# Performance work log

Measured on AMD Instinct MI355X. Metric: run time of the kernel, lower is better.

Reference implementation:

```python
import jax, jax.numpy as jnp
import numpy as np

B, L, H, NH = 2, 512, 128, 2
DH = H // NH
POS_VOCAB, REL_VOCAB = 512, 257


def setup_inputs() -> dict:
    key = jax.random.key(0)
    ks = jax.random.split(key, 16)
    s = 0.02
    inp = {
        "query": jax.random.normal(ks[0], (B, L, H), jnp.float32),
        "key": jax.random.normal(ks[1], (B, L, H), jnp.float32),
        "value": jax.random.normal(ks[2], (B, L, H), jnp.float32),
        "Wq": jax.random.normal(ks[3], (H, H), jnp.float32) * s,
        "bq": jnp.zeros((H,), jnp.float32),
        "Wk": jax.random.normal(ks[4], (H, H), jnp.float32) * s,
        "bk": jnp.zeros((H,), jnp.float32),
        "Wv": jax.random.normal(ks[5], (H, H), jnp.float32) * s,
        "bv": jnp.zeros((H,), jnp.float32),
        "Wo": jax.random.normal(ks[6], (H, H), jnp.float32) * s,
        "bo": jnp.zeros((H,), jnp.float32),
        "E_PK": jax.random.normal(ks[7], (POS_VOCAB, H), jnp.float32) * s,
        "E_PV": jax.random.normal(ks[8], (POS_VOCAB, H), jnp.float32) * s,
        "E_RK": jax.random.normal(ks[9], (REL_VOCAB, H), jnp.float32) * s,
        "E_RV": jax.random.normal(ks[10], (REL_VOCAB, H), jnp.float32) * s,
        "poss_seq": jax.random.randint(ks[11], (B, L), 0, POS_VOCAB),
        "interval_seq": jax.random.randint(ks[12], (B, L, L), 0, REL_VOCAB),
        # causal mask (True = attend), same role as attn_mask in the torch module
        "attn_mask": jnp.broadcast_to(jnp.tril(jnp.ones((L, L), bool)), (B, L, L)),
    }
    return inp


def reference(query, key, value, Wq, bq, Wk, bk, Wv, bv, Wo, bo,
              E_PK, E_PV, E_RK, E_RV, poss_seq, interval_seq, attn_mask):
    b, l, _ = query.shape
    # linear projections (torch Linear: x @ W.T + b)
    Q = query @ Wq.T + bq
    K = key @ Wk.T + bk + E_PK[poss_seq]
    V = value @ Wv.T + bv + E_PV[poss_seq]
    # relative key/value embeddings: (b, l, l, h, dh) -> (b, h, l, l, dh)
    rel_k = E_RK[interval_seq].reshape(b, l, l, NH, DH).transpose(0, 3, 1, 2, 4)
    rel_v = E_RV[interval_seq].reshape(b, l, l, NH, DH).transpose(0, 3, 1, 2, 4)
    # split heads: (b, h, l, dh)
    Qh = Q.reshape(b, l, NH, DH).transpose(0, 2, 1, 3)
    Kh = K.reshape(b, l, NH, DH).transpose(0, 2, 1, 3)
    Vh = V.reshape(b, l, NH, DH).transpose(0, 2, 1, 3)
    scores = jnp.einsum('bhld,bhkd->bhlk', Qh, Kh)
    scores = scores + jnp.einsum('bhld,bhlkd->bhlk', Qh, rel_k)
    scores = scores / jnp.sqrt(jnp.float32(DH))
    m = attn_mask[:, None]  # (b, 1, l, l)
    scores = jnp.where(m, scores, -jnp.inf)
    w = jax.nn.softmax(scores, axis=-1)
    w = jnp.where(m, w, 0.0)
    out = jnp.einsum('bhlk,bhkd->bhld', w, Vh)
    out = out + jnp.einsum('bhlk,bhlkd->bhld', w, rel_v)
    out = out.transpose(0, 2, 1, 3).reshape(b, l, H)
    out = out @ Wo.T + bo
    out = jnp.where(jnp.isnan(out), 0.0, out)
    return out
```

## Files before the change

### kernel.cpp

```cpp
#include <hip/hip_runtime.h>
#include <math.h>

#define LL 512
#define HH 128
#define NHH 2
#define DHH 64
#define RELV 257

#define OFF_QH   0
#define OFF_KT   131072
#define OFF_VH   262144
#define OFF_PK   393216
#define OFF_WQT  919552
#define OFF_WKT  935936
#define OFF_WVT  952320
#define OFF_WOT  968704
#define OFF_ERKT 985088

__global__ void prep_kernel(const float* Wq, const float* Wk, const float* Wv,
                            const float* Wo, const float* E_RK, float* ws) {
    int g = blockIdx.x * 256 + threadIdx.x;
    if (g < 65536) {
        int m = g >> 14, rem = g & 16383, i = rem >> 7, j = rem & 127;
        const float* W = (m == 0) ? Wq : (m == 1) ? Wk : (m == 2) ? Wv : Wo;
        ws[OFF_WQT + m * 16384 + i * 128 + j] = W[j * 128 + i];
    } else if (g < 65536 + 128 * RELV) {
        int g2 = g - 65536;
        int hd = g2 / RELV, r = g2 - hd * RELV;
        ws[OFF_ERKT + hd * RELV + r] = E_RK[r * HH + hd];
    }
}

__launch_bounds__(256)
__global__ void qkv_kernel(const float* q_in, const float* k_in, const float* v_in,
                           const float* bq, const float* bk, const float* bv,
                           const float* E_PK, const float* E_PV, const int* poss,
                           const float* Wqt, const float* Wkt, const float* Wvt,
                           const float* ERKt,
                           float* Qh, float* Kt, float* Vh, float* PK) {
    int row = blockIdx.x;
    int b = row >> 9, l = row & 511;
    int t = threadIdx.x;
    int j = t & 127, half = t >> 7;

    __shared__ float xin[3][128];
    __shared__ float pp[3][2][128];
    __shared__ float qrow[128];

    for (int g = t; g < 384; g += 256) {
        int m = g >> 7, i = g & 127;
        const float* src = (m == 0) ? q_in : (m == 1) ? k_in : v_in;
        xin[m][i] = src[row * 128 + i];
    }
    __syncthreads();

    float aq = 0.f, ak = 0.f, av = 0.f;
    int i0 = half * 64;
#pragma unroll 8
    for (int i = i0; i < i0 + 64; i++) {
        float xq = xin[0][i], xk = xin[1][i], xv = xin[2][i];
        aq += xq * Wqt[i * 128 + j];
        ak += xk * Wkt[i * 128 + j];
        av += xv * Wvt[i * 128 + j];
    }
    pp[0][half][j] = aq; pp[1][half][j] = ak; pp[2][half][j] = av;
    __syncthreads();

    if (t < 128) {
        int pos = poss[row];
        float q = pp[0][0][j] + pp[0][1][j] + bq[j];
        float k = pp[1][0][j] + pp[1][1][j] + bk[j] + E_PK[pos * 128 + j];
        float v = pp[2][0][j] + pp[2][1][j] + bv[j] + E_PV[pos * 128 + j];
        int h = j >> 6, d = j & 63, bh = b * NHH + h;
        Qh[(bh * LL + l) * DHH + d] = q;
        Vh[(bh * LL + l) * DHH + d] = v;
        Kt[(bh * DHH + d) * LL + l] = k;
        qrow[j] = q;
    }
    __syncthreads();

    int h = t >> 7, rr = t & 127;
    const float* qh = qrow + h * DHH;
    for (int r = rr; r < RELV; r += 128) {
        float acc = 0.f;
        const float* er = ERKt + h * DHH * RELV + r;
#pragma unroll 8
        for (int dd = 0; dd < DHH; dd++) acc += qh[dd] * er[dd * RELV];
        PK[((b * NHH + h) * LL + l) * RELV + r] = acc;
    }
}

__launch_bounds__(256)
__global__ void attn_kernel(const float* Qh, const float* Kt, const float* Vh,
                            const float* PK, const float* E_RV,
                            const float* Wot, const float* bo,
                            const int* interval, float* out) {
    int blk = blockIdx.x;
    int b = blk & 1;
    int l = 511 - (blk >> 1);
    int t = threadIdx.x;
    int w = t >> 6, lane = t & 63;
    int h = w >> 1, kseg = w & 1;
    int bh = b * NHH + h;
    int nk = l + 1;
    int kmid = (((nk + 1) >> 1) + 3) & ~3;
    int kbase = kseg ? kmid : 0;
    int kend  = kseg ? nk : (kmid < nk ? kmid : nk);

    __shared__ float q4[4][DHH];
    __shared__ float pks[4][RELV];
    __shared__ float wb[4][RELV];
    __shared__ __align__(16) float sc[4][256];
    __shared__ float oa[4][DHH];
    __shared__ float po[2][HH];
    __shared__ float reds[4];

    q4[w][lane] = Qh[(bh * LL + l) * DHH + lane];
    const float* PKrow = PK + (bh * LL + l) * RELV;
#pragma unroll
    for (int c = 0; c < 4; c++) {
        pks[w][lane + c * 64] = PKrow[lane + c * 64];
        wb[w][lane + c * 64] = 0.f;
    }
    if (lane == 0) { pks[w][256] = PKrow[256]; wb[w][256] = 0.f; }
    __syncthreads();

    int k0 = kbase + lane * 4;
    float4 a4 = make_float4(0.f, 0.f, 0.f, 0.f);
    int4 idx4 = make_int4(0, 0, 0, 0);
    const int* idxr = interval + (b * LL + l) * LL;
    if (k0 < kend) {
        idx4 = ((const int4*)idxr)[k0 >> 2];
        const float* kb = Kt + bh * DHH * LL + k0;
#pragma unroll 16
        for (int d = 0; d < DHH; d++) {
            float4 kk = *(const float4*)(kb + d * LL);
            float qd = q4[w][d];
            a4.x += qd * kk.x; a4.y += qd * kk.y;
            a4.z += qd * kk.z; a4.w += qd * kk.w;
        }
    }
    float e0 = (k0 + 0 < kend) ? __expf((a4.x + pks[w][idx4.x]) * 0.125f) : 0.f;
    float e1 = (k0 + 1 < kend) ? __expf((a4.y + pks[w][idx4.y]) * 0.125f) : 0.f;
    float e2 = (k0 + 2 < kend) ? __expf((a4.z + pks[w][idx4.z]) * 0.125f) : 0.f;
    float e3 = (k0 + 3 < kend) ? __expf((a4.w + pks[w][idx4.w]) * 0.125f) : 0.f;

    float ss = (e0 + e1) + (e2 + e3);
#pragma unroll
    for (int off = 32; off > 0; off >>= 1) ss += __shfl_down(ss, off);
    if (lane == 0) reds[w] = ss;
    __syncthreads();
    float inv = 1.f / (reds[h * 2] + reds[h * 2 + 1]);

    float w0 = e0 * inv, w1 = e1 * inv, w2 = e2 * inv, w3 = e3 * inv;
    *(float4*)&sc[w][lane * 4] = make_float4(w0, w1, w2, w3);
    if (k0 + 0 < kend) atomicAdd(&wb[w][idx4.x], w0);
    if (k0 + 1 < kend) atomicAdd(&wb[w][idx4.y], w1);
    if (k0 + 2 < kend) atomicAdd(&wb[w][idx4.z], w2);
    if (k0 + 3 < kend) atomicAdd(&wb[w][idx4.w], w3);
    __syncthreads();

    float acc0 = 0.f, acc1 = 0.f, acc2 = 0.f, acc3 = 0.f;
    const float* vb = Vh + bh * LL * DHH + lane;
    int kcnt = kend - kbase; if (kcnt < 0) kcnt = 0;
    int niter = (kcnt + 3) >> 2;
    for (int ci = 0; ci < niter; ci++) {
        int k = kbase + ci * 4;
        const float* scw = sc[w] + ci * 4;
        acc0 += scw[0] * vb[(k + 0) * DHH];
        acc1 += scw[1] * vb[(k + 1) * DHH];
        acc2 += scw[2] * vb[(k + 2) * DHH];
        acc3 += scw[3] * vb[(k + 3) * DHH];
    }

    const float* ev = E_RV + h * DHH + lane;
    const float* wbA = wb[h * 2];
    const float* wbB = wb[h * 2 + 1];
    int r = kseg ? 128 : 0;
    int r1 = kseg ? RELV : 128;
    for (; r + 4 <= r1; r += 4) {
        acc0 += (wbA[r + 0] + wbB[r + 0]) * ev[(r + 0) * HH];
        acc1 += (wbA[r + 1] + wbB[r + 1]) * ev[(r + 1) * HH];
        acc2 += (wbA[r + 2] + wbB[r + 2]) * ev[(r + 2) * HH];
        acc3 += (wbA[r + 3] + wbB[r + 3]) * ev[(r + 3) * HH];
    }
    for (; r < r1; r++) acc0 += (wbA[r] + wbB[r]) * ev[r * HH];

    oa[w][lane] = (acc0 + acc1) + (acc2 + acc3);
    __syncthreads();

    int j = t & 127, half = t >> 7;
    const float* oaA = oa[half * 2];
    const float* oaB = oa[half * 2 + 1];
    int i0 = half * 64;
    float pa = 0.f, pb = 0.f;
#pragma unroll 8
    for (int ii = 0; ii < 64; ii += 2) {
        float a0 = oaA[ii] + oaB[ii];
        float a1 = oaA[ii + 1] + oaB[ii + 1];
        pa += a0 * Wot[(i0 + ii) * HH + j];
        pb += a1 * Wot[(i0 + ii + 1) * HH + j];
    }
    po[half][j] = pa + pb;
    __syncthreads();
    if (t < HH) {
        float o = po[0][t] + po[1][t] + bo[t];
        if (isnan(o)) o = 0.f;
        out[(b * LL + l) * HH + t] = o;
    }
}

extern "C" void kernel_launch(void* const* d_in, const int* in_sizes, int n_in,
                              void* d_out, int out_size, void* d_ws, size_t ws_size,
                              hipStream_t stream) {
    const float* query = (const float*)d_in[0];
    const float* key   = (const float*)d_in[1];
    const float* value = (const float*)d_in[2];
    const float* Wq = (const float*)d_in[3];  const float* bq = (const float*)d_in[4];
    const float* Wk = (const float*)d_in[5];  const float* bk = (const float*)d_in[6];
    const float* Wv = (const float*)d_in[7];  const float* bv = (const float*)d_in[8];
    const float* Wo = (const float*)d_in[9];  const float* bo = (const float*)d_in[10];
    const float* E_PK = (const float*)d_in[11];
    const float* E_PV = (const float*)d_in[12];
    const float* E_RK = (const float*)d_in[13];
    const float* E_RV = (const float*)d_in[14];
    const int* poss     = (const int*)d_in[15];
    const int* interval = (const int*)d_in[16];

    float* ws = (float*)d_ws;
    float* Qh  = ws + OFF_QH;
    float* Kt  = ws + OFF_KT;
    float* Vh  = ws + OFF_VH;
    float* PK  = ws + OFF_PK;
    float* Wqt = ws + OFF_WQT;
    float* Wkt = ws + OFF_WKT;
    float* Wvt = ws + OFF_WVT;
    float* Wot = ws + OFF_WOT;
    float* ERKt = ws + OFF_ERKT;
    float* out = (float*)d_out;

    prep_kernel<<<385, 256, 0, stream>>>(Wq, Wk, Wv, Wo, E_RK, ws);
    qkv_kernel<<<1024, 256, 0, stream>>>(query, key, value, bq, bk, bv,
                                         E_PK, E_PV, poss, Wqt, Wkt, Wvt, ERKt,
                                         Qh, Kt, Vh, PK);
    attn_kernel<<<1024, 256, 0, stream>>>(Qh, Kt, Vh, PK, E_RV, Wot, bo,
                                          interval, out);
}
```

Baseline: 142.2 us.

## Split attention epilogue into separate kernel and batch rows for weight reuse

```diff
diff --git a/kernel.cpp b/kernel.cpp
--- a/kernel.cpp
+++ b/kernel.cpp
@@ -11,11 +11,14 @@
 #define OFF_KT   131072
 #define OFF_VH   262144
 #define OFF_PK   393216
-#define OFF_WQT  919552
-#define OFF_WKT  935936
-#define OFF_WVT  952320
-#define OFF_WOT  968704
-#define OFF_ERKT 985088
+#define OFF_OA   919552
+#define OFF_WB   1181696
+#define OFF_SUMS 1708032
+#define OFF_WQT  1712128
+#define OFF_WKT  1728512
+#define OFF_WVT  1744896
+#define OFF_WOT  1761280
+#define OFF_ERKT 1777664
 
 __global__ void prep_kernel(const float* Wq, const float* Wk, const float* Wv,
                             const float* Wo, const float* E_RK, float* ws) {
@@ -38,126 +41,132 @@
                            const float* Wqt, const float* Wkt, const float* Wvt,
                            const float* ERKt,
                            float* Qh, float* Kt, float* Vh, float* PK) {
-    int row = blockIdx.x;
-    int b = row >> 9, l = row & 511;
+    int row0 = blockIdx.x * 2;
+    int b = row0 >> 9;
+    int l0 = row0 & 511;
     int t = threadIdx.x;
+
+    __shared__ float xin[3][2][128];
+    __shared__ float pp[3][2][2][128];
+    __shared__ float qr[2][128];
+
+    for (int g = t; g < 768; g += 256) {
+        int m = g >> 8, rem = g & 255, rr = rem >> 7, i = rem & 127;
+        const float* src = (m == 0) ? q_in : (m == 1) ? k_in : v_in;
+        xin[m][rr][i] = src[(row0 + rr) * 128 + i];
+    }
+    __syncthreads();
+
     int j = t & 127, half = t >> 7;
-
-    __shared__ float xin[3][128];
-    __shared__ float pp[3][2][128];
-    __shared__ float qrow[128];
-
-    for (int g = t; g < 384; g += 256) {
-        int m = g >> 7, i = g & 127;
-        const float* src = (m == 0) ? q_in : (m == 1) ? k_in : v_in;
-        xin[m][i] = src[row * 128 + i];
-    }
-    __syncthreads();
-
-    float aq = 0.f, ak = 0.f, av = 0.f;
+    float aq0 = 0, ak0 = 0, av0 = 0, aq1 = 0, ak1 = 0, av1 = 0;
     int i0 = half * 64;
 #pragma unroll 8
     for (int i = i0; i < i0 + 64; i++) {
-        float xq = xin[0][i], xk = xin[1][i], xv = xin[2][i];
-        aq += xq * Wqt[i * 128 + j];
-        ak += xk * Wkt[i * 128 + j];
-        av += xv * Wvt[i * 128 + j];
-    }
-    pp[0][half][j] = aq; pp[1][half][j] = ak; pp[2][half][j] = av;
-    __syncthreads();
-
-    if (t < 128) {
+        float wq = Wqt[i * 128 + j], wk = Wkt[i * 128 + j], wv = Wvt[i * 128 + j];
+        aq0 += xin[0][0][i] * wq; aq1 += xin[0][1][i] * wq;
+        ak0 += xin[1][0][i] * wk; ak1 += xin[1][1][i] * wk;
+        av0 += xin[2][0][i] * wv; av1 += xin[2][1][i] * wv;
+    }
+    pp[0][0][half][j] = aq0; pp[0][1][half][j] = aq1;
+    pp[1][0][half][j] = ak0; pp[1][1][half][j] = ak1;
+    pp[2][0][half][j] = av0; pp[2][1][half][j] = av1;
+    __syncthreads();
+
+    {
+        int rr = t >> 7;
+        int row = row0 + rr, l = l0 + rr;
         int pos = poss[row];
-        float q = pp[0][0][j] + pp[0][1][j] + bq[j];
-        float k = pp[1][0][j] + pp[1][1][j] + bk[j] + E_PK[pos * 128 + j];
-        float v = pp[2][0][j] + pp[2][1][j] + bv[j] + E_PV[pos * 128 + j];
+        float q = pp[0][rr][0][j] + pp[0][rr][1][j] + bq[j];
+        float k = pp[1][rr][0][j] + pp[1][rr][1][j] + bk[j] + E_PK[pos * 128 + j];
+        float v = pp[2][rr][0][j] + pp[2][rr][1][j] + bv[j] + E_PV[pos * 128 + j];
         int h = j >> 6, d = j & 63, bh = b * NHH + h;
         Qh[(bh * LL + l) * DHH + d] = q;
         Vh[(bh * LL + l) * DHH + d] = v;
         Kt[(bh * DHH + d) * LL + l] = k;
-        qrow[j] = q;
-    }
-    __syncthreads();
-
-    int h = t >> 7, rr = t & 127;
-    const float* qh = qrow + h * DHH;
-    for (int r = rr; r < RELV; r += 128) {
-        float acc = 0.f;
-        const float* er = ERKt + h * DHH * RELV + r;
+        qr[rr][j] = q;
+    }
+    __syncthreads();
+
+    int h = t >> 7, rl = t & 127;
+    const float* qh0 = qr[0] + h * 64;
+    const float* qh1 = qr[1] + h * 64;
+    const float* erb = ERKt + h * 64 * RELV;
+    float* pk0 = PK + ((b * NHH + h) * LL + l0) * RELV;
+    float* pk1 = pk0 + RELV;
+#pragma unroll
+    for (int pass = 0; pass < 3; pass++) {
+        int r = rl + pass * 128;
+        if (r < RELV) {
+            float a0 = 0.f, a1 = 0.f;
 #pragma unroll 8
-        for (int dd = 0; dd < DHH; dd++) acc += qh[dd] * er[dd * RELV];
-        PK[((b * NHH + h) * LL + l) * RELV + r] = acc;
-    }
-}
-
-__launch_bounds__(256)
+            for (int dd = 0; dd < 64; dd++) {
+                float er = erb[dd * RELV + r];
+                a0 += qh0[dd] * er; a1 += qh1[dd] * er;
+            }
+            pk0[r] = a0; pk1[r] = a1;
+        }
+    }
+}
+
+__launch_bounds__(128)
 __global__ void attn_kernel(const float* Qh, const float* Kt, const float* Vh,
-                            const float* PK, const float* E_RV,
-                            const float* Wot, const float* bo,
-                            const int* interval, float* out) {
+                            const float* PK, const int* interval,
+                            float* OAg, float* WBg, float* SUMSg) {
     int blk = blockIdx.x;
-    int b = blk & 1;
-    int l = 511 - (blk >> 1);
+    int h = blk & 1;
+    int i = blk >> 1;
+    int b = i & 1;
+    int l = 511 - (i >> 1);
+    int bh = b * NHH + h;
+    int r_out = b * LL + l;
+    int nk = l + 1;
     int t = threadIdx.x;
-    int w = t >> 6, lane = t & 63;
-    int h = w >> 1, kseg = w & 1;
-    int bh = b * NHH + h;
-    int nk = l + 1;
+    int seg = t >> 6, lane = t & 63;
+
+    __shared__ float q2[DHH];
+    __shared__ float pks[RELV];
+    __shared__ float wb[RELV];
+    __shared__ __align__(16) float sc[2][256];
+
+    if (t < 64) q2[t] = Qh[(bh * LL + l) * DHH + t];
+    const float* PKrow = PK + (bh * LL + l) * RELV;
+    for (int idx = t; idx < RELV; idx += 128) { pks[idx] = PKrow[idx]; wb[idx] = 0.f; }
+    __syncthreads();
+
     int kmid = (((nk + 1) >> 1) + 3) & ~3;
-    int kbase = kseg ? kmid : 0;
-    int kend  = kseg ? nk : (kmid < nk ? kmid : nk);
-
-    __shared__ float q4[4][DHH];
-    __shared__ float pks[4][RELV];
-    __shared__ float wb[4][RELV];
-    __shared__ __align__(16) float sc[4][256];
-    __shared__ float oa[4][DHH];
-    __shared__ float po[2][HH];
-    __shared__ float reds[4];
-
-    q4[w][lane] = Qh[(bh * LL + l) * DHH + lane];
-    const float* PKrow = PK + (bh * LL + l) * RELV;
-#pragma unroll
-    for (int c = 0; c < 4; c++) {
-        pks[w][lane + c * 64] = PKrow[lane + c * 64];
-        wb[w][lane + c * 64] = 0.f;
-    }
-    if (lane == 0) { pks[w][256] = PKrow[256]; wb[w][256] = 0.f; }
-    __syncthreads();
+    int kbase = seg ? kmid : 0;
+    int kend  = seg ? nk : (kmid < nk ? kmid : nk);
 
     int k0 = kbase + lane * 4;
     float4 a4 = make_float4(0.f, 0.f, 0.f, 0.f);
     int4 idx4 = make_int4(0, 0, 0, 0);
     const int* idxr = interval + (b * LL + l) * LL;
     if (k0 < kend) {
-        idx4 = ((const int4*)idxr)[k0 >> 2];
+        idx4 = *(const int4*)(idxr + k0);
         const float* kb = Kt + bh * DHH * LL + k0;
 #pragma unroll 16
         for (int d = 0; d < DHH; d++) {
             float4 kk = *(const float4*)(kb + d * LL);
-            float qd = q4[w][d];
+            float qd = q2[d];
             a4.x += qd * kk.x; a4.y += qd * kk.y;
             a4.z += qd * kk.z; a4.w += qd * kk.w;
         }
     }
-    float e0 = (k0 + 0 < kend) ? __expf((a4.x + pks[w][idx4.x]) * 0.125f) : 0.f;
-    float e1 = (k0 + 1 < kend) ? __expf((a4.y + pks[w][idx4.y]) * 0.125f) : 0.f;
-    float e2 = (k0 + 2 < kend) ? __expf((a4.z + pks[w][idx4.z]) * 0.125f) : 0.f;
-    float e3 = (k0 + 3 < kend) ? __expf((a4.w + pks[w][idx4.w]) * 0.125f) : 0.f;
+    float e0 = (k0 + 0 < kend) ? __expf((a4.x + pks[idx4.x]) * 0.125f) : 0.f;
+    float e1 = (k0 + 1 < kend) ? __expf((a4.y + pks[idx4.y]) * 0.125f) : 0.f;
+    float e2 = (k0 + 2 < kend) ? __expf((a4.z + pks[idx4.z]) * 0.125f) : 0.f;
+    float e3 = (k0 + 3 < kend) ? __expf((a4.w + pks[idx4.w]) * 0.125f) : 0.f;
 
     float ss = (e0 + e1) + (e2 + e3);
 #pragma unroll
     for (int off = 32; off > 0; off >>= 1) ss += __shfl_down(ss, off);
-    if (lane == 0) reds[w] = ss;
-    __syncthreads();
-    float inv = 1.f / (reds[h * 2] + reds[h * 2 + 1]);
-
-    float w0 = e0 * inv, w1 = e1 * inv, w2 = e2 * inv, w3 = e3 * inv;
-    *(float4*)&sc[w][lane * 4] = make_float4(w0, w1, w2, w3);
-    if (k0 + 0 < kend) atomicAdd(&wb[w][idx4.x], w0);
-    if (k0 + 1 < kend) atomicAdd(&wb[w][idx4.y], w1);
-    if (k0 + 2 < kend) atomicAdd(&wb[w][idx4.z], w2);
-    if (k0 + 3 < kend) atomicAdd(&wb[w][idx4.w], w3);
+    if (lane == 0) SUMSg[r_out * 4 + h * 2 + seg] = ss;
+
+    *(float4*)&sc[seg][lane * 4] = make_float4(e0, e1, e2, e3);
+    if (k0 + 0 < kend) atomicAdd(&wb[idx4.x], e0);
+    if (k0 + 1 < kend) atomicAdd(&wb[idx4.y], e1);
+    if (k0 + 2 < kend) atomicAdd(&wb[idx4.z], e2);
+    if (k0 + 3 < kend) atomicAdd(&wb[idx4.w], e3);
     __syncthreads();
 
     float acc0 = 0.f, acc1 = 0.f, acc2 = 0.f, acc3 = 0.f;
@@ -166,47 +175,93 @@
     int niter = (kcnt + 3) >> 2;
     for (int ci = 0; ci < niter; ci++) {
         int k = kbase + ci * 4;
-        const float* scw = sc[w] + ci * 4;
+        const float* scw = sc[seg] + ci * 4;
         acc0 += scw[0] * vb[(k + 0) * DHH];
         acc1 += scw[1] * vb[(k + 1) * DHH];
         acc2 += scw[2] * vb[(k + 2) * DHH];
         acc3 += scw[3] * vb[(k + 3) * DHH];
     }
-
-    const float* ev = E_RV + h * DHH + lane;
-    const float* wbA = wb[h * 2];
-    const float* wbB = wb[h * 2 + 1];
-    int r = kseg ? 128 : 0;
-    int r1 = kseg ? RELV : 128;
-    for (; r + 4 <= r1; r += 4) {
-        acc0 += (wbA[r + 0] + wbB[r + 0]) * ev[(r + 0) * HH];
-        acc1 += (wbA[r + 1] + wbB[r + 1]) * ev[(r + 1) * HH];
-        acc2 += (wbA[r + 2] + wbB[r + 2]) * ev[(r + 2) * HH];
-        acc3 += (wbA[r + 3] + wbB[r + 3]) * ev[(r + 3) * HH];
-    }
-    for (; r < r1; r++) acc0 += (wbA[r] + wbB[r]) * ev[r * HH];
-
-    oa[w][lane] = (acc0 + acc1) + (acc2 + acc3);
-    __syncthreads();
-
-    int j = t & 127, half = t >> 7;
-    const float* oaA = oa[half * 2];
-    const float* oaB = oa[half * 2 + 1];
-    int i0 = half * 64;
-    float pa = 0.f, pb = 0.f;
+    OAg[r_out * 256 + (h * 2 + seg) * 64 + lane] = (acc0 + acc1) + (acc2 + acc3);
+    for (int idx = t; idx < RELV; idx += 128)
+        WBg[(r_out * 2 + h) * RELV + idx] = wb[idx];
+}
+
+__launch_bounds__(256)
+__global__ void epi_kernel(const float* OAg, const float* WBg, const float* SUMSg,
+                           const float* E_RV, const float* Wot, const float* bo,
+                           float* out) {
+    int row0 = blockIdx.x * 4;
+    int t = threadIdx.x;
+
+    __shared__ float wbL[4][2 * RELV];
+    __shared__ float oaRaw[4][256];
+    __shared__ float oaL[4][128];
+    __shared__ float pa[2][4][128];
+    __shared__ float pp2[2][4][128];
+    __shared__ float sL[16];
+
+    if (t < 16) sL[t] = SUMSg[row0 * 4 + t];
+    for (int g = t; g < 1024; g += 256) {
+        int ro = g >> 8, jj = g & 255;
+        oaRaw[ro][jj] = OAg[(row0 + ro) * 256 + jj];
+    }
+#pragma unroll
+    for (int ro = 0; ro < 4; ro++)
+        for (int idx = t; idx < 2 * RELV; idx += 256)
+            wbL[ro][idx] = WBg[(row0 + ro) * 2 * RELV + idx];
+    __syncthreads();
+
+    for (int g = t; g < 512; g += 256) {
+        int ro = g >> 7, hd = g & 127, hh = hd >> 6, dd = hd & 63;
+        float inv = 1.f / (sL[ro * 4 + hh * 2] + sL[ro * 4 + hh * 2 + 1]);
+        oaL[ro][hd] = (oaRaw[ro][hh * 128 + dd] + oaRaw[ro][hh * 128 + 64 + dd]) * inv;
+    }
+
+    int rp = t >> 7, h = (t >> 6) & 1, d = t & 63;
+    float ac0 = 0.f, ac1 = 0.f, ac2 = 0.f, ac3 = 0.f;
+    int rA = rp ? 128 : 0;
+    int rB = rp ? RELV : 128;
+    const float* ev = E_RV + h * 64 + d;
+    for (int r = rA; r < rB; r++) {
+        float e = ev[r * HH];
+        ac0 += wbL[0][h * RELV + r] * e;
+        ac1 += wbL[1][h * RELV + r] * e;
+        ac2 += wbL[2][h * RELV + r] * e;
+        ac3 += wbL[3][h * RELV + r] * e;
+    }
+    {
+        int hd = h * 64 + d;
+        float i0 = 1.f / (sL[0  + h * 2] + sL[0  + h * 2 + 1]);
+        float i1 = 1.f / (sL[4  + h * 2] + sL[4  + h * 2 + 1]);
+        float i2 = 1.f / (sL[8  + h * 2] + sL[8  + h * 2 + 1]);
+        float i3 = 1.f / (sL[12 + h * 2] + sL[12 + h * 2 + 1]);
+        pa[rp][0][hd] = ac0 * i0; pa[rp][1][hd] = ac1 * i1;
+        pa[rp][2][hd] = ac2 * i2; pa[rp][3][hd] = ac3 * i3;
+    }
+    __syncthreads();
+
+    int j = t & 127, ip = t >> 7;
+    float p0 = 0.f, p1 = 0.f, p2 = 0.f, p3 = 0.f;
+    int ib = ip * 64;
 #pragma unroll 8
-    for (int ii = 0; ii < 64; ii += 2) {
-        float a0 = oaA[ii] + oaB[ii];
-        float a1 = oaA[ii + 1] + oaB[ii + 1];
-        pa += a0 * Wot[(i0 + ii) * HH + j];
-        pb += a1 * Wot[(i0 + ii + 1) * HH + j];
-    }
-    po[half][j] = pa + pb;
-    __syncthreads();
-    if (t < HH) {
-        float o = po[0][t] + po[1][t] + bo[t];
+    for (int ii = 0; ii < 64; ii++) {
+        int i = ib + ii;
+        float wv = Wot[i * 128 + j];
+        float a0 = oaL[0][i] + pa[0][0][i] + pa[1][0][i];
+        float a1 = oaL[1][i] + pa[0][1][i] + pa[1][1][i];
+        float a2 = oaL[2][i] + pa[0][2][i] + pa[1][2][i];
+        float a3 = oaL[3][i] + pa[0][3][i] + pa[1][3][i];
+        p0 += a0 * wv; p1 += a1 * wv; p2 += a2 * wv; p3 += a3 * wv;
+    }
+    pp2[ip][0][j] = p0; pp2[ip][1][j] = p1;
+    pp2[ip][2][j] = p2; pp2[ip][3][j] = p3;
+    __syncthreads();
+
+    for (int g = t; g < 512; g += 256) {
+        int ro = g >> 7, jj = g & 127;
+        float o = pp2[0][ro][jj] + pp2[1][ro][jj] + bo[jj];
         if (isnan(o)) o = 0.f;
-        out[(b * LL + l) * HH + t] = o;
+        out[(row0 + ro) * 128 + jj] = o;
     }
 }
 
@@ -228,21 +283,24 @@
     const int* interval = (const int*)d_in[16];
 
     float* ws = (float*)d_ws;
-    float* Qh  = ws + OFF_QH;
-    float* Kt  = ws + OFF_KT;
-    float* Vh  = ws + OFF_VH;
-    float* PK  = ws + OFF_PK;
-    float* Wqt = ws + OFF_WQT;
-    float* Wkt = ws + OFF_WKT;
-    float* Wvt = ws + OFF_WVT;
-    float* Wot = ws + OFF_WOT;
+    float* Qh   = ws + OFF_QH;
+    float* Kt   = ws + OFF_KT;
+    float* Vh   = ws + OFF_VH;
+    float* PK   = ws + OFF_PK;
+    float* OA   = ws + OFF_OA;
+    float* WB   = ws + OFF_WB;
+    float* SUMS = ws + OFF_SUMS;
+    float* Wqt  = ws + OFF_WQT;
+    float* Wkt  = ws + OFF_WKT;
+    float* Wvt  = ws + OFF_WVT;
+    float* Wot  = ws + OFF_WOT;
     float* ERKt = ws + OFF_ERKT;
     float* out = (float*)d_out;
 
     prep_kernel<<<385, 256, 0, stream>>>(Wq, Wk, Wv, Wo, E_RK, ws);
-    qkv_kernel<<<1024, 256, 0, stream>>>(query, key, value, bq, bk, bv,
-                                         E_PK, E_PV, poss, Wqt, Wkt, Wvt, ERKt,
-                                         Qh, Kt, Vh, PK);
-    attn_kernel<<<1024, 256, 0, stream>>>(Qh, Kt, Vh, PK, E_RV, Wot, bo,
-                                          interval, out);
-}
+    qkv_kernel<<<512, 256, 0, stream>>>(query, key, value, bq, bk, bv,
+                                        E_PK, E_PV, poss, Wqt, Wkt, Wvt, ERKt,
+                                        Qh, Kt, Vh, PK);
+    attn_kernel<<<2048, 128, 0, stream>>>(Qh, Kt, Vh, PK, interval, OA, WB, SUMS);
+    epi_kernel<<<256, 256, 0, stream>>>(OA, WB, SUMS, E_RV, Wot, bo, out);
+}
```

Measured after the change: 181.6 us. 27.7% more time.
